# Optimization experiments

Hardware: AMD Instinct MI355X
Metric: run time of the kernel (lower is better)

## Reference

```python
import jax, jax.numpy as jnp
import numpy as np

B, S, D = 2, 2048, 2048
H, DP = 16, 128
WINDOW = 512


def setup_inputs() -> dict:
    key = jax.random.key(0)
    ks = jax.random.split(key, 9)
    sc = 0.02
    return {
        "x": jax.random.normal(ks[0], (B, S, D), dtype=jnp.float32),
        "wq": jax.random.normal(ks[1], (D, H * DP), dtype=jnp.float32) * sc,
        "bq": jax.random.normal(ks[2], (H * DP,), dtype=jnp.float32) * sc,
        "wk": jax.random.normal(ks[3], (D, H * DP), dtype=jnp.float32) * sc,
        "bk": jax.random.normal(ks[4], (H * DP,), dtype=jnp.float32) * sc,
        "wv": jax.random.normal(ks[5], (D, H * DP), dtype=jnp.float32) * sc,
        "bv": jax.random.normal(ks[6], (H * DP,), dtype=jnp.float32) * sc,
        "wo": jax.random.normal(ks[7], (H * DP,), dtype=jnp.float32) * sc,
        "bo": jax.random.normal(ks[8], (1,), dtype=jnp.float32) * sc,
    }


def _sliding_window_mask(seq_len, window):
    q_idx = jnp.arange(seq_len)[:, None]
    kv_idx = jnp.arange(seq_len)[None, :]
    return (q_idx >= kv_idx) & (q_idx - kv_idx < window)


def reference(x, wq, bq, wk, bk, wv, bv, wo, bo):
    b, s, _ = x.shape
    # QKV projections -> (B, H, S, DP)
    q = (x @ wq + bq).reshape(b, s, H, DP).transpose(0, 2, 1, 3)
    k = (x @ wk + bk).reshape(b, s, H, DP).transpose(0, 2, 1, 3)
    v = (x @ wv + bv).reshape(b, s, H, DP).transpose(0, 2, 1, 3)
    scale = 1.0 / np.sqrt(DP).astype(np.float32)
    scores = jnp.einsum("bhqd,bhkd->bhqk", q, k) * scale  # (B,H,S,S)
    mask = _sliding_window_mask(s, WINDOW)
    scores = jnp.where(mask, scores, jnp.finfo(scores.dtype).min)
    attn = jax.nn.softmax(scores, axis=-1)
    o = jnp.einsum("bhqk,bhkd->bhqd", attn, v)  # (B,H,S,DP)
    o = o.transpose(0, 2, 1, 3).reshape(b, s, H * DP)
    return o @ wo + bo[0]  # (B, S)
```

## Files before the change

### kernel.cpp

```cpp
#include <hip/hip_runtime.h>

typedef unsigned short USH;
typedef __bf16 v8bf __attribute__((ext_vector_type(8)));
typedef float v4f __attribute__((ext_vector_type(4)));
typedef unsigned short us8 __attribute__((ext_vector_type(8)));

#define SB 2048
#define DD 2048
#define NH 16
#define DPH 128

__device__ __forceinline__ USH f2bf(float f) {
  unsigned u = __float_as_uint(f);
  u = u + 0x7fffu + ((u >> 16) & 1u);
  return (USH)(u >> 16);
}

#define GL16(gp, lp)                                                   \
  __builtin_amdgcn_global_load_lds(                                    \
      (const __attribute__((address_space(1))) void*)(gp),             \
      (__attribute__((address_space(3))) void*)(lp), 16, 0, 0)

__global__ __launch_bounds__(256) void k_prep(const float* __restrict__ x,
    const float* __restrict__ wq, const float* __restrict__ wk,
    const float* __restrict__ wvf, const float* __restrict__ bvf,
    const float* __restrict__ wo,
    USH* __restrict__ xb, USH* __restrict__ wqt, USH* __restrict__ wkt,
    USH* __restrict__ wvoT, float* __restrict__ bvo) {
  __shared__ USH tl[64][72];
  __shared__ float red[256];
  const int bid = blockIdx.x;
  const int t = threadIdx.x;
  if (bid < 4096) {
    const int i = (bid * 256 + t) * 8;
    const float4 a = *(const float4*)&x[i];
    const float4 b = *(const float4*)&x[i + 4];
    v8bf o;
    o[0] = (__bf16)a.x; o[1] = (__bf16)a.y; o[2] = (__bf16)a.z; o[3] = (__bf16)a.w;
    o[4] = (__bf16)b.x; o[5] = (__bf16)b.y; o[6] = (__bf16)b.z; o[7] = (__bf16)b.w;
    *(v8bf*)&xb[i] = o;
  } else if (bid < 6144) {
    const int rel = bid - 4096;
    const int z = rel >> 10, rem = rel & 1023;
    const float* w = z ? wk : wq;
    USH* wt = z ? wkt : wqt;
    const int k0 = (rem >> 5) * 64, j0 = (rem & 31) * 64;
#pragma unroll
    for (int p = 0; p < 4; ++p) {
      const int r = p * 16 + (t >> 4);
      const int c = (t & 15) * 4;
      const float4 v = *(const float4*)&w[(size_t)(k0 + r) * DD + j0 + c];
      tl[c + 0][r] = f2bf(v.x);
      tl[c + 1][r] = f2bf(v.y);
      tl[c + 2][r] = f2bf(v.z);
      tl[c + 3][r] = f2bf(v.w);
    }
    __syncthreads();
#pragma unroll
    for (int p = 0; p < 2; ++p) {
      const int j = p * 32 + (t >> 3);
      const int seg = (t & 7) * 8;
      us8 v = *(const us8*)&tl[j][seg];
      *(us8*)&wt[(size_t)(j0 + j) * DD + k0 + seg] = v;
    }
  } else {
    const int d = bid - 6144;
    const float* src = (d == DD) ? bvf : (wvf + (size_t)d * DD);
    const float4 a0 = *(const float4*)&src[t * 8];
    const float4 a1 = *(const float4*)&src[t * 8 + 4];
    const float4 w0 = *(const float4*)&wo[t * 8];
    const float4 w1 = *(const float4*)&wo[t * 8 + 4];
    red[t] = a0.x * w0.x + a0.y * w0.y + a0.z * w0.z + a0.w * w0.w +
             a1.x * w1.x + a1.y * w1.y + a1.z * w1.z + a1.w * w1.w;
    __syncthreads();
    for (int s = 8; s > 0; s >>= 1) {
      if ((t & 15) < s) red[t] += red[t + s];
      __syncthreads();
    }
    if ((t & 15) == 0) {
      if (d == DD) bvo[t >> 4] = red[t];
      else wvoT[(size_t)(t >> 4) * DD + d] = f2bf(red[t]);
    }
  }
}

__global__ __launch_bounds__(64) void k_vw2(const USH* __restrict__ xb,
    const USH* __restrict__ wvoT, const float* __restrict__ bvo,
    float* __restrict__ vw) {
  const int lane = threadIdx.x & 63;
  const int lr = lane & 15, g = lane >> 4;
  const int r0 = blockIdx.x * 16;
  v4f acc = (v4f){0.f, 0.f, 0.f, 0.f};
  const USH* ap = xb + (size_t)(r0 + lr) * DD + g * 8;
  const USH* bp = wvoT + (size_t)lr * DD + g * 8;
#pragma unroll 4
  for (int kt = 0; kt < 64; ++kt) {
    v8bf af = *(const v8bf*)(ap + kt * 32);
    v8bf bf = *(const v8bf*)(bp + kt * 32);
    acc = __builtin_amdgcn_mfma_f32_16x16x32_bf16(af, bf, acc, 0, 0, 0);
  }
  const float bb = bvo[lr];
#pragma unroll
  for (int rr = 0; rr < 4; ++rr) {
    const int row = r0 + g * 4 + rr;
    vw[((size_t)(row >> 11) * NH + lr) * SB + (row & 2047)] = acc[rr] + bb;
  }
}

__global__ __launch_bounds__(512, 2) void k_gemm256(
    const USH* __restrict__ xb,
    const USH* __restrict__ wqt, const USH* __restrict__ wkt,
    const float* __restrict__ bq, const float* __restrict__ bk,
    USH* __restrict__ Qb, USH* __restrict__ Kb) {
  __shared__ USH As[2][16384];
  __shared__ USH Bs[2][16384];
  const int fid = blockIdx.x;
  const int nid = (fid & 7) * 32 + (fid >> 3);
  const int z = nid >> 7;
  const int ty = (nid >> 3) & 15, tx = nid & 7;
  const int row0 = ty * 256, col0 = tx * 256;
  const USH* wt = z ? wkt : wqt;
  const float* bias = z ? bk : bq;
  USH* outp = z ? Kb : Qb;
  const float qscale = z ? 1.0f : 0.08838834764831845f;
  const int t = threadIdx.x;
  const int w = t >> 6, lane = t & 63;
  const int lr = lane & 15, g = lane >> 4;
  const int wr = w >> 2, wc = w & 3;
  size_t gA[4], gB[4];
  int ldsOff[4];
#pragma unroll
  for (int q = 0; q < 4; ++q) {
    const int p = q * 512 + t;
    const int row = p >> 3, ps = p & 7;
    const int sl = ps ^ (row & 7);
    gA[q] = (size_t)(row0 + row) * DD + sl * 8;
    gB[q] = (size_t)(col0 + row) * DD + sl * 8;
    ldsOff[q] = p * 8;
  }
  const int swz = (g ^ (lr & 7)) * 8;
  const int k1o = swz ^ 32;
  const int rowA = wr * 128 + lr;
  const int rowB = wc * 64 + lr;

  v4f acc[8][4];
#pragma unroll
  for (int i = 0; i < 8; ++i)
#pragma unroll
    for (int j = 0; j < 4; ++j) acc[i][j] = (v4f){0.f, 0.f, 0.f, 0.f};

#pragma unroll
  for (int q = 0; q < 4; ++q) {
    GL16(xb + gA[q], &As[0][ldsOff[q]]);
    GL16(wt + gB[q], &Bs[0][ldsOff[q]]);
  }
#pragma unroll
  for (int q = 0; q < 4; ++q) {
    GL16(xb + gA[q] + 64, &As[1][ldsOff[q]]);
    GL16(wt + gB[q] + 64, &Bs[1][ldsOff[q]]);
  }
  asm volatile("s_waitcnt vmcnt(8)" ::: "memory");
  __builtin_amdgcn_s_barrier();
  __builtin_amdgcn_sched_barrier(0);

  v8bf bfr0[4], bfr1[4], af0[4], af4[4], af1[4], af5[4];
#pragma unroll
  for (int ni = 0; ni < 4; ++ni)
    bfr0[ni] = *(const v8bf*)&Bs[0][(rowB + ni * 16) * 64 + swz];
#pragma unroll
  for (int mi = 0; mi < 4; ++mi)
    af0[mi] = *(const v8bf*)&As[0][(rowA + mi * 16) * 64 + swz];

  for (int kt = 0; kt < 32; ++kt) {
    const int c = kt & 1;
    const USH* Ab = &As[c][0];
    const USH* Bb = &Bs[c][0];
    __builtin_amdgcn_sched_barrier(0);
#pragma unroll
    for (int mi = 0; mi < 4; ++mi)
      af4[mi] = *(const v8bf*)&Ab[(rowA + (mi + 4) * 16) * 64 + swz];
    asm volatile("s_waitcnt lgkmcnt(4)" ::: "memory");
    __builtin_amdgcn_sched_barrier(0);
    __builtin_amdgcn_s_setprio(1);
#pragma unroll
    for (int mi = 0; mi < 4; ++mi)
#pragma unroll
      for (int ni = 0; ni < 4; ++ni)
        acc[mi][ni] = __builtin_amdgcn_mfma_f32_16x16x32_bf16(af0[mi], bfr0[ni], acc[mi][ni], 0, 0, 0);
    __builtin_amdgcn_s_setprio(0);
    __builtin_amdgcn_s_barrier();
    __builtin_amdgcn_sched_barrier(0);
#pragma unroll
    for (int ni = 0; ni < 4; ++ni)
      bfr1[ni] = *(const v8bf*)&Bb[(rowB + ni * 16) * 64 + k1o];
#pragma unroll
    for (int mi = 0; mi < 4; ++mi)
      af1[mi] = *(const v8bf*)&Ab[(rowA + mi * 16) * 64 + k1o];
    asm volatile("s_waitcnt lgkmcnt(8)" ::: "memory");
    __builtin_amdgcn_sched_barrier(0);
    __builtin_amdgcn_s_setprio(1);
#pragma unroll
    for (int mi = 0; mi < 4; ++mi)
#pragma unroll
      for (int ni = 0; ni < 4; ++ni)
        acc[mi + 4][ni] = __builtin_amdgcn_mfma_f32_16x16x32_bf16(af4[mi], bfr0[ni], acc[mi + 4][ni], 0, 0, 0);
    __builtin_amdgcn_s_setprio(0);
    __builtin_amdgcn_s_barrier();
    __builtin_amdgcn_sched_barrier(0);
#pragma unroll
    for (int mi = 0; mi < 4; ++mi)
      af5[mi] = *(const v8bf*)&Ab[(rowA + (mi + 4) * 16) * 64 + k1o];
    asm volatile("s_waitcnt lgkmcnt(4)" ::: "memory");
    __builtin_amdgcn_sched_barrier(0);
    __builtin_amdgcn_s_setprio(1);
#pragma unroll
    for (int mi = 0; mi < 4; ++mi)
#pragma unroll
      for (int ni = 0; ni < 4; ++ni)
        acc[mi][ni] = __builtin_amdgcn_mfma_f32_16x16x32_bf16(af1[mi], bfr1[ni], acc[mi][ni], 0, 0, 0);
    __builtin_amdgcn_s_setprio(0);
    __builtin_amdgcn_s_barrier();
    asm volatile("s_waitcnt lgkmcnt(0)" ::: "memory");
    __builtin_amdgcn_sched_barrier(0);
    __builtin_amdgcn_s_barrier();
    if (kt < 30) {
      const size_t ko = (size_t)(kt + 2) * 64;
#pragma unroll
      for (int q = 0; q < 4; ++q) {
        GL16(xb + gA[q] + ko, &As[c][ldsOff[q]]);
        GL16(wt + gB[q] + ko, &Bs[c][ldsOff[q]]);
      }
    }
    __builtin_amdgcn_s_setprio(1);
#pragma unroll
    for (int mi = 0; mi < 4; ++mi)
#pragma unroll
      for (int ni = 0; ni < 4; ++ni)
        acc[mi + 4][ni] = __builtin_amdgcn_mfma_f32_16x16x32_bf16(af5[mi], bfr1[ni], acc[mi + 4][ni], 0, 0, 0);
    __builtin_amdgcn_s_setprio(0);
    if (kt < 31) {
      if (kt < 30) {
        asm volatile("s_waitcnt vmcnt(8)" ::: "memory");
      } else {
        asm volatile("s_waitcnt vmcnt(0)" ::: "memory");
      }
      __builtin_amdgcn_s_barrier();
      __builtin_amdgcn_sched_barrier(0);
      const USH* An = &As[c ^ 1][0];
      const USH* Bn = &Bs[c ^ 1][0];
#pragma unroll
      for (int ni = 0; ni < 4; ++ni)
        bfr0[ni] = *(const v8bf*)&Bn[(rowB + ni * 16) * 64 + swz];
#pragma unroll
      for (int mi = 0; mi < 4; ++mi)
        af0[mi] = *(const v8bf*)&An[(rowA + mi * 16) * 64 + swz];
    }
  }

#pragma unroll
  for (int ni = 0; ni < 4; ++ni) {
    const int col = col0 + wc * 64 + ni * 16 + lr;
    const float bv_ = bias[col];
    const int hh = col >> 7, dp = col & 127;
#pragma unroll
    for (int mi = 0; mi < 8; ++mi) {
#pragma unroll
      for (int rr = 0; rr < 4; ++rr) {
        const int row = row0 + wr * 128 + mi * 16 + g * 4 + rr;
        const int bi = row >> 11, s = row & 2047;
        outp[(((size_t)bi * NH + hh) * SB + s) * DPH + dp] =
            f2bf((acc[mi][ni][rr] + bv_) * qscale);
      }
    }
  }
}

__global__ __launch_bounds__(512) void k_attn(const USH* __restrict__ Qb,
    const USH* __restrict__ Kb, const float* __restrict__ vw,
    float* __restrict__ part) {
  __shared__ USH Ks[2][8192];
  const int bh = blockIdx.y;
  const int t = threadIdx.x;
  const int wid = t >> 6, lane = t & 63;
  const int lr = lane & 15, g = lane >> 4;
  const int qblk = blockIdx.x * 128;
  const int qb = qblk + wid * 16;
  const USH* Qp = Qb + (size_t)bh * SB * DPH;
  const USH* Kp = Kb + (size_t)bh * SB * DPH;
  const float* vwp = vw + (size_t)bh * SB;

  v8bf qf[4];
  {
    const USH* qrp = Qp + (size_t)(qb + lr) * DPH + g * 8;
#pragma unroll
    for (int kc = 0; kc < 4; ++kc) qf[kc] = *(const v8bf*)(qrp + kc * 32);
  }
  size_t srcO[2];
  int ldsO[2];
#pragma unroll
  for (int q = 0; q < 2; ++q) {
    const int r = t >> 3, ps = t & 7;
    srcO[q] = (size_t)r * DPH + q * 64 + (size_t)(((ps ^ (r & 7)) * 8));
    ldsO[q] = (q * 512 + t) * 8;
  }

  float m[4], ls[4], os[4];
#pragma unroll
  for (int r = 0; r < 4; ++r) { m[r] = -1e30f; ls[r] = 0.f; os[r] = 0.f; }

  const int kb0 = qblk > 511 ? qblk - 512 : 0;
  const int kbend = qblk + 64;

  GL16(Kp + (size_t)kb0 * DPH + srcO[0], &Ks[0][ldsO[0]]);
  GL16(Kp + (size_t)kb0 * DPH + srcO[1], &Ks[0][ldsO[1]]);
  __syncthreads();

  int buf = 0;
  for (int kb = kb0; kb <= kbend; kb += 64, buf ^= 1) {
    if (kb < kbend) {
      GL16(Kp + (size_t)(kb + 64) * DPH + srcO[0], &Ks[buf ^ 1][ldsO[0]]);
      GL16(Kp + (size_t)(kb + 64) * DPH + srcO[1], &Ks[buf ^ 1][ldsO[1]]);
    }
    const USH* base = &Ks[buf][0];
    v4f acc[4];
    float vv[4];
#pragma unroll
    for (int i = 0; i < 4; ++i) {
      v4f a = (v4f){0.f, 0.f, 0.f, 0.f};
#pragma unroll
      for (int kc = 0; kc < 4; ++kc) {
        const int lrow = (kc >> 1) * 64 + i * 16 + lr;
        v8bf kf = *(const v8bf*)&base[lrow * 64 + ((((kc & 1) * 4 + g) ^ (lr & 7)) * 8)];
        a = __builtin_amdgcn_mfma_f32_16x16x32_bf16(qf[kc], kf, a, 0, 0, 0);
      }
      acc[i] = a;
      vv[i] = vwp[kb + i * 16 + lr];
    }
#pragma unroll
    for (int r = 0; r < 4; ++r) {
      const int q_i = qb + g * 4 + r;
      const int k0i = kb + lr;
      float sc0 = acc[0][r], sc1 = acc[1][r], sc2 = acc[2][r], sc3 = acc[3][r];
      sc0 = (k0i <= q_i && q_i - k0i < 512) ? sc0 : -1e30f;
      sc1 = (k0i + 16 <= q_i && q_i - (k0i + 16) < 512) ? sc1 : -1e30f;
      sc2 = (k0i + 32 <= q_i && q_i - (k0i + 32) < 512) ? sc2 : -1e30f;
      sc3 = (k0i + 48 <= q_i && q_i - (k0i + 48) < 512) ? sc3 : -1e30f;
      float rm = fmaxf(fmaxf(sc0, sc1), fmaxf(sc2, sc3));
      rm = fmaxf(rm, __shfl_xor(rm, 1));
      rm = fmaxf(rm, __shfl_xor(rm, 2));
      rm = fmaxf(rm, __shfl_xor(rm, 4));
      rm = fmaxf(rm, __shfl_xor(rm, 8));
      const float mn = fmaxf(m[r], rm);
      const float al = __expf(m[r] - mn);
      const float p0 = __expf(sc0 - mn);
      const float p1 = __expf(sc1 - mn);
      const float p2 = __expf(sc2 - mn);
      const float p3 = __expf(sc3 - mn);
      ls[r] = ls[r] * al + (p0 + p1 + p2 + p3);
      os[r] = os[r] * al + (p0 * vv[0] + p1 * vv[1] + p2 * vv[2] + p3 * vv[3]);
      m[r] = mn;
    }
    __syncthreads();
  }
#pragma unroll
  for (int r = 0; r < 4; ++r) {
    os[r] += __shfl_xor(os[r], 1); ls[r] += __shfl_xor(ls[r], 1);
    os[r] += __shfl_xor(os[r], 2); ls[r] += __shfl_xor(ls[r], 2);
    os[r] += __shfl_xor(os[r], 4); ls[r] += __shfl_xor(ls[r], 4);
    os[r] += __shfl_xor(os[r], 8); ls[r] += __shfl_xor(ls[r], 8);
  }
  if (lr == 0) {
#pragma unroll
    for (int r = 0; r < 4; ++r)
      part[(size_t)bh * SB + qb + g * 4 + r] = os[r] / ls[r];
  }
}

__global__ __launch_bounds__(256) void k_final(const float* __restrict__ part,
    const float* __restrict__ bo, float* __restrict__ out) {
  const int i = blockIdx.x * 256 + threadIdx.x;
  const int b = i >> 11, s = i & 2047;
  float acc = bo[0];
#pragma unroll
  for (int h = 0; h < NH; ++h) acc += part[(size_t)(b * NH + h) * SB + s];
  out[i] = acc;
}

extern "C" void kernel_launch(void* const* d_in, const int* in_sizes, int n_in,
                              void* d_out, int out_size, void* d_ws, size_t ws_size,
                              hipStream_t stream) {
  const float* x   = (const float*)d_in[0];
  const float* wq  = (const float*)d_in[1];
  const float* bq  = (const float*)d_in[2];
  const float* wk  = (const float*)d_in[3];
  const float* bk  = (const float*)d_in[4];
  const float* wvf = (const float*)d_in[5];
  const float* bvf = (const float*)d_in[6];
  const float* wo  = (const float*)d_in[7];
  const float* bo  = (const float*)d_in[8];
  float* out = (float*)d_out;
  char* ws = (char*)d_ws;

  USH*   wqt = (USH*)(ws);
  USH*   wkt = (USH*)(ws + 8388608);
  USH*   Qb  = (USH*)(ws + 16777216);
  USH*   Kb  = (USH*)(ws + 33554432);
  float* vw  = (float*)(ws + 50331648);
  USH*   wvoT= (USH*)(ws + 50593792);
  float* bvo = (float*)(ws + 50724864);
  float* part= (float*)(ws + 50725120);
  USH*   xbf = (USH*)(ws + 50987264);

  k_prep<<<dim3(8193), dim3(256), 0, stream>>>(x, wq, wk, wvf, bvf, wo,
                                               xbf, wqt, wkt, wvoT, bvo);
  k_vw2<<<dim3(256), dim3(64), 0, stream>>>(xbf, wvoT, bvo, vw);
  k_gemm256<<<dim3(256), dim3(512), 0, stream>>>(xbf, wqt, wkt, bq, bk, Qb, Kb);
  k_attn<<<dim3(16, 32), dim3(512), 0, stream>>>(Qb, Kb, vw, part);
  k_final<<<dim3(16), dim3(256), 0, stream>>>(part, bo, out);
}
```

Before: 132.7 us.

## Restructure QK projection GEMM to triple-buffered K=32 stages with split-K LDS layout

The 256x256 QK projection GEMM changes from double-buffered 64-wide K tiles to triple-buffered 32-wide K tiles. The LDS layout now packs two 32-column K halves into one 64-element row, and different warp groups read different halves via the swizzle. Global-to-LDS loads for stage k+2 are issued at the start of each iteration, split around the MFMA blocks, so the loads overlap compute with fewer barriers per stage. The cost is twice as many loop iterations and smaller stages, which lowers MFMA work per barrier.

```diff
diff --git a/kernel.cpp b/kernel.cpp
--- a/kernel.cpp
+++ b/kernel.cpp
@@ -112,8 +112,8 @@
     const USH* __restrict__ wqt, const USH* __restrict__ wkt,
     const float* __restrict__ bq, const float* __restrict__ bk,
     USH* __restrict__ Qb, USH* __restrict__ Kb) {
-  __shared__ USH As[2][16384];
-  __shared__ USH Bs[2][16384];
+  __shared__ USH As[3][8192];
+  __shared__ USH Bs[3][8192];
   const int fid = blockIdx.x;
   const int nid = (fid & 7) * 32 + (fid >> 3);
   const int z = nid >> 7;
@@ -127,21 +127,27 @@
   const int w = t >> 6, lane = t & 63;
   const int lr = lane & 15, g = lane >> 4;
   const int wr = w >> 2, wc = w & 3;
-  size_t gA[4], gB[4];
-  int ldsOff[4];
-#pragma unroll
-  for (int q = 0; q < 4; ++q) {
+  size_t gA[2], gB[2];
+  int ldsO[2];
+#pragma unroll
+  for (int q = 0; q < 2; ++q) {
     const int p = q * 512 + t;
-    const int row = p >> 3, ps = p & 7;
-    const int sl = ps ^ (row & 7);
-    gA[q] = (size_t)(row0 + row) * DD + sl * 8;
-    gB[q] = (size_t)(col0 + row) * DD + sl * 8;
-    ldsOff[q] = p * 8;
-  }
-  const int swz = (g ^ (lr & 7)) * 8;
-  const int k1o = swz ^ 32;
-  const int rowA = wr * 128 + lr;
-  const int rowB = wc * 64 + lr;
+    const int L = p >> 3, sp = p & 7;
+    const int j = sp ^ (L & 7);
+    const int srow = L + (j >> 2) * 128;
+    const int scol = (j & 3) * 8;
+    gA[q] = (size_t)(row0 + srow) * DD + scol;
+    gB[q] = (size_t)(col0 + srow) * DD + scol;
+    ldsO[q] = p * 8;
+  }
+  int offA[8], offB[4];
+#pragma unroll
+  for (int mi = 0; mi < 8; ++mi)
+    offA[mi] = (lr + mi * 16) * 64 + (((g + 4 * wr) ^ (lr & 7)) * 8);
+#pragma unroll
+  for (int ni = 0; ni < 4; ++ni)
+    offB[ni] = ((wc & 1) * 64 + lr + ni * 16) * 64 +
+               (((g + 4 * (wc >> 1)) ^ (lr & 7)) * 8);
 
   v4f acc[8][4];
 #pragma unroll
@@ -149,36 +155,35 @@
 #pragma unroll
     for (int j = 0; j < 4; ++j) acc[i][j] = (v4f){0.f, 0.f, 0.f, 0.f};
 
-#pragma unroll
-  for (int q = 0; q < 4; ++q) {
-    GL16(xb + gA[q], &As[0][ldsOff[q]]);
-    GL16(wt + gB[q], &Bs[0][ldsOff[q]]);
-  }
-#pragma unroll
-  for (int q = 0; q < 4; ++q) {
-    GL16(xb + gA[q] + 64, &As[1][ldsOff[q]]);
-    GL16(wt + gB[q] + 64, &Bs[1][ldsOff[q]]);
-  }
-  asm volatile("s_waitcnt vmcnt(8)" ::: "memory");
+  GL16(xb + gA[0], &As[0][ldsO[0]]);
+  GL16(xb + gA[1], &As[0][ldsO[1]]);
+  GL16(wt + gB[0], &Bs[0][ldsO[0]]);
+  GL16(wt + gB[1], &Bs[0][ldsO[1]]);
+  GL16(xb + gA[0] + 32, &As[1][ldsO[0]]);
+  GL16(xb + gA[1] + 32, &As[1][ldsO[1]]);
+  GL16(wt + gB[0] + 32, &Bs[1][ldsO[0]]);
+  GL16(wt + gB[1] + 32, &Bs[1][ldsO[1]]);
+  asm volatile("s_waitcnt vmcnt(4)" ::: "memory");
   __builtin_amdgcn_s_barrier();
   __builtin_amdgcn_sched_barrier(0);
 
-  v8bf bfr0[4], bfr1[4], af0[4], af4[4], af1[4], af5[4];
-#pragma unroll
-  for (int ni = 0; ni < 4; ++ni)
-    bfr0[ni] = *(const v8bf*)&Bs[0][(rowB + ni * 16) * 64 + swz];
-#pragma unroll
-  for (int mi = 0; mi < 4; ++mi)
-    af0[mi] = *(const v8bf*)&As[0][(rowA + mi * 16) * 64 + swz];
-
-  for (int kt = 0; kt < 32; ++kt) {
-    const int c = kt & 1;
-    const USH* Ab = &As[c][0];
-    const USH* Bb = &Bs[c][0];
-    __builtin_amdgcn_sched_barrier(0);
+  v8bf af0[4], af4[4], bfr[4];
+#pragma unroll
+  for (int ni = 0; ni < 4; ++ni) bfr[ni] = *(const v8bf*)&Bs[0][offB[ni]];
+#pragma unroll
+  for (int mi = 0; mi < 4; ++mi) af0[mi] = *(const v8bf*)&As[0][offA[mi]];
+
+  int c = 0;
+  for (int kt = 0; kt < 64; ++kt) {
+    const int n2 = (c == 0) ? 2 : c - 1;
+    const size_t ko = (size_t)(kt + 2) * 32;
+    if (kt < 62) {
+      GL16(xb + gA[0] + ko, &As[n2][ldsO[0]]);
+      GL16(xb + gA[1] + ko, &As[n2][ldsO[1]]);
+    }
 #pragma unroll
     for (int mi = 0; mi < 4; ++mi)
-      af4[mi] = *(const v8bf*)&Ab[(rowA + (mi + 4) * 16) * 64 + swz];
+      af4[mi] = *(const v8bf*)&As[c][offA[mi + 4]];
     asm volatile("s_waitcnt lgkmcnt(4)" ::: "memory");
     __builtin_amdgcn_sched_barrier(0);
     __builtin_amdgcn_s_setprio(1);
@@ -186,74 +191,36 @@
     for (int mi = 0; mi < 4; ++mi)
 #pragma unroll
       for (int ni = 0; ni < 4; ++ni)
-        acc[mi][ni] = __builtin_amdgcn_mfma_f32_16x16x32_bf16(af0[mi], bfr0[ni], acc[mi][ni], 0, 0, 0);
+        acc[mi][ni] = __builtin_amdgcn_mfma_f32_16x16x32_bf16(af0[mi], bfr[ni], acc[mi][ni], 0, 0, 0);
     __builtin_amdgcn_s_setprio(0);
     __builtin_amdgcn_s_barrier();
-    __builtin_amdgcn_sched_barrier(0);
-#pragma unroll
-    for (int ni = 0; ni < 4; ++ni)
-      bfr1[ni] = *(const v8bf*)&Bb[(rowB + ni * 16) * 64 + k1o];
-#pragma unroll
-    for (int mi = 0; mi < 4; ++mi)
-      af1[mi] = *(const v8bf*)&Ab[(rowA + mi * 16) * 64 + k1o];
-    asm volatile("s_waitcnt lgkmcnt(8)" ::: "memory");
+    if (kt < 62) {
+      GL16(wt + gB[0] + ko, &Bs[n2][ldsO[0]]);
+      GL16(wt + gB[1] + ko, &Bs[n2][ldsO[1]]);
+    }
+    asm volatile("s_waitcnt lgkmcnt(0)" ::: "memory");
     __builtin_amdgcn_sched_barrier(0);
     __builtin_amdgcn_s_setprio(1);
 #pragma unroll
     for (int mi = 0; mi < 4; ++mi)
 #pragma unroll
       for (int ni = 0; ni < 4; ++ni)
-        acc[mi + 4][ni] = __builtin_amdgcn_mfma_f32_16x16x32_bf16(af4[mi], bfr0[ni], acc[mi + 4][ni], 0, 0, 0);
+        acc[mi + 4][ni] = __builtin_amdgcn_mfma_f32_16x16x32_bf16(af4[mi], bfr[ni], acc[mi + 4][ni], 0, 0, 0);
     __builtin_amdgcn_s_setprio(0);
-    __builtin_amdgcn_s_barrier();
-    __builtin_amdgcn_sched_barrier(0);
-#pragma unroll
-    for (int mi = 0; mi < 4; ++mi)
-      af5[mi] = *(const v8bf*)&Ab[(rowA + (mi + 4) * 16) * 64 + k1o];
-    asm volatile("s_waitcnt lgkmcnt(4)" ::: "memory");
-    __builtin_amdgcn_sched_barrier(0);
-    __builtin_amdgcn_s_setprio(1);
-#pragma unroll
-    for (int mi = 0; mi < 4; ++mi)
-#pragma unroll
-      for (int ni = 0; ni < 4; ++ni)
-        acc[mi][ni] = __builtin_amdgcn_mfma_f32_16x16x32_bf16(af1[mi], bfr1[ni], acc[mi][ni], 0, 0, 0);
-    __builtin_amdgcn_s_setprio(0);
-    __builtin_amdgcn_s_barrier();
-    asm volatile("s_waitcnt lgkmcnt(0)" ::: "memory");
-    __builtin_amdgcn_sched_barrier(0);
-    __builtin_amdgcn_s_barrier();
-    if (kt < 30) {
-      const size_t ko = (size_t)(kt + 2) * 64;
-#pragma unroll
-      for (int q = 0; q < 4; ++q) {
-        GL16(xb + gA[q] + ko, &As[c][ldsOff[q]]);
-        GL16(wt + gB[q] + ko, &Bs[c][ldsOff[q]]);
-      }
-    }
-    __builtin_amdgcn_s_setprio(1);
-#pragma unroll
-    for (int mi = 0; mi < 4; ++mi)
-#pragma unroll
-      for (int ni = 0; ni < 4; ++ni)
-        acc[mi + 4][ni] = __builtin_amdgcn_mfma_f32_16x16x32_bf16(af5[mi], bfr1[ni], acc[mi + 4][ni], 0, 0, 0);
-    __builtin_amdgcn_s_setprio(0);
-    if (kt < 31) {
-      if (kt < 30) {
-        asm volatile("s_waitcnt vmcnt(8)" ::: "memory");
+    if (kt < 63) {
+      if (kt < 62) {
+        asm volatile("s_waitcnt vmcnt(4)" ::: "memory");
       } else {
         asm volatile("s_waitcnt vmcnt(0)" ::: "memory");
       }
       __builtin_amdgcn_s_barrier();
       __builtin_amdgcn_sched_barrier(0);
-      const USH* An = &As[c ^ 1][0];
-      const USH* Bn = &Bs[c ^ 1][0];
-#pragma unroll
-      for (int ni = 0; ni < 4; ++ni)
-        bfr0[ni] = *(const v8bf*)&Bn[(rowB + ni * 16) * 64 + swz];
-#pragma unroll
-      for (int mi = 0; mi < 4; ++mi)
-        af0[mi] = *(const v8bf*)&An[(rowA + mi * 16) * 64 + swz];
+      const int cn = (c == 2) ? 0 : c + 1;
+#pragma unroll
+      for (int ni = 0; ni < 4; ++ni) bfr[ni] = *(const v8bf*)&Bs[cn][offB[ni]];
+#pragma unroll
+      for (int mi = 0; mi < 4; ++mi) af0[mi] = *(const v8bf*)&As[cn][offA[mi]];
+      c = cn;
     }
   }
 
```

After: 143.0 us. +7.8%, slower.
